# Kernel optimization log

Measured on AMD Instinct MI355X. Metric: run time of the kernel, lower is better.

The kernel has to match this reference:

```python
import jax, jax.numpy as jnp
import numpy as np

B, S, HID, NH = 2, 2048, 2048, 16
HD = HID // NH  # head_dim = 128


def setup_inputs() -> dict:
    key = jax.random.key(0)
    ks = jax.random.split(key, 10)
    sc = 1.0 / np.sqrt(HID)
    inp = {
        "hidden_state": jax.random.normal(ks[0], (B, S, HID), dtype=jnp.float32),
        # upper-triangular (strict) causal mask: 1 where attention is forbidden
        "casual_mask": jnp.triu(jnp.ones((S, S), dtype=jnp.float32), k=1),
        # pad last 128 tokens of each sequence
        "pad_mask": jnp.concatenate(
            [jnp.zeros((B, S - 128), jnp.float32), jnp.ones((B, 128), jnp.float32)], axis=1
        ),
        # weights stored [in, out] (transposed vs torch Linear)
        "Wq": jax.random.normal(ks[1], (HID, HID), dtype=jnp.float32) * sc,
        "bq": jnp.zeros((HID,), jnp.float32),
        "Wk": jax.random.normal(ks[2], (HID, HD), dtype=jnp.float32) * sc,
        "bk": jnp.zeros((HD,), jnp.float32),
        "Wv": jax.random.normal(ks[3], (HID, HD), dtype=jnp.float32) * sc,
        "bv": jnp.zeros((HD,), jnp.float32),
        "Wo": jax.random.normal(ks[4], (HID, HID), dtype=jnp.float32) * sc,
        "bo": jnp.zeros((HID,), jnp.float32),
    }
    return inp


def reference(hidden_state, casual_mask, pad_mask, Wq, bq, Wk, bk, Wv, bv, Wo, bo):
    bsz, seq_len, hid = hidden_state.shape
    nh = NH
    hd = hid // nh
    q = hidden_state @ Wq + bq                      # [B,S,HID]
    k = hidden_state @ Wk + bk                      # [B,S,HD]  single shared head
    v = hidden_state @ Wv + bv                      # [B,S,HD]
    q = q.reshape(bsz, seq_len, nh, hd).transpose(0, 2, 1, 3)  # [B,NH,S,HD]
    # attn scores: shared K broadcast across all query heads
    scores = jnp.einsum("bhqd,bkd->bhqk", q, k) / jnp.sqrt(jnp.float32(hd))
    scores = scores + casual_mask * (-1e9)
    scores = scores + pad_mask[:, None, None, :] * (-1e9)
    probs = jax.nn.softmax(scores, axis=-1)         # [B,NH,S,S]
    out = jnp.einsum("bhqk,bkd->bhqd", probs, v)    # [B,NH,S,HD]
    out = out.transpose(0, 2, 1, 3).reshape(bsz, seq_len, hid)
    return out @ Wo + bo
```

## Files before the change

### kernel.cpp

```cpp
#include <hip/hip_runtime.h>
#include <hip/hip_bf16.h>
#include <math.h>

#define B_    2
#define S_    2048
#define HID_  2048
#define NH_   16
#define HD_   128
#define MTOT  4096
#define QKV_N 2304

typedef short bf16x8 __attribute__((ext_vector_type(8)));
typedef float f32x4  __attribute__((ext_vector_type(4)));
typedef float f32x16 __attribute__((ext_vector_type(16)));

__device__ __forceinline__ ushort f2bf(float f) {
    __hip_bfloat16 h = __float2bfloat16(f);
    ushort u; __builtin_memcpy(&u, &h, 2); return u;
}

__device__ __forceinline__ void gload_lds16(const void* g, void* l) {
    __builtin_amdgcn_global_load_lds(
        (const __attribute__((address_space(1))) void*)g,
        (__attribute__((address_space(3))) void*)l, 16, 0, 0);
}
__device__ __forceinline__ void gload_lds4(const void* g, void* l) {
    __builtin_amdgcn_global_load_lds(
        (const __attribute__((address_space(1))) void*)g,
        (__attribute__((address_space(3))) void*)l, 4, 0, 0);
}

__global__ void cast_f32_bf16(const float* __restrict__ in, ushort* __restrict__ out)
{
    long i = ((long)blockIdx.x * 256 + threadIdx.x) * 8;
    float4 a = *(const float4*)&in[i];
    float4 b = *(const float4*)&in[i + 4];
    uint4 o;
    o.x = (uint)f2bf(a.x) | ((uint)f2bf(a.y) << 16);
    o.y = (uint)f2bf(a.z) | ((uint)f2bf(a.w) << 16);
    o.z = (uint)f2bf(b.x) | ((uint)f2bf(b.y) << 16);
    o.w = (uint)f2bf(b.z) | ((uint)f2bf(b.w) << 16);
    *(uint4*)&out[i] = o;
}

__global__ void transcast(const float* __restrict__ W, ushort* __restrict__ T,
                          int N, int rowoff)
{
    __shared__ float tile[32][33];
    const int tx = threadIdx.x & 31, ty = threadIdx.x >> 5;
    const int n0 = blockIdx.x * 32, k0 = blockIdx.y * 32;
#pragma unroll
    for (int i = 0; i < 4; i++)
        tile[ty + 8 * i][tx] = W[(long)(k0 + ty + 8 * i) * N + n0 + tx];
    __syncthreads();
#pragma unroll
    for (int i = 0; i < 4; i++)
        T[(long)(rowoff + n0 + ty + 8 * i) * 2048 + k0 + tx] = f2bf(tile[tx][ty + 8 * i]);
}

__global__ void fuse_bias(const float* __restrict__ bq, const float* __restrict__ bk,
                          const float* __restrict__ bv, float* __restrict__ bqkv)
{
    int i = blockIdx.x * 256 + threadIdx.x;
    if (i < 2048)      bqkv[i] = bq[i];
    else if (i < 2176) bqkv[i] = bk[i - 2048];
    else if (i < QKV_N) bqkv[i] = bv[i - 2176];
}

__global__ __launch_bounds__(256, 2) void gemm_qkv(
    const ushort* __restrict__ A, const ushort* __restrict__ Bt,
    const float* __restrict__ bias,
    ushort* __restrict__ qbuf, ushort* __restrict__ kbuf,
    ushort* __restrict__ vtbuf)
{
    const int K = HID_;
    __shared__ __align__(16) ushort As[128 * 32];
    __shared__ __align__(16) ushort Bs[128 * 32];
    const int t = threadIdx.x;
    const int w = t >> 6, l = t & 63;
    const long bm = (long)blockIdx.y * 128;
    const long bn = (long)blockIdx.x * 128;

    f32x4 acc[4][4];
#pragma unroll
    for (int i = 0; i < 4; i++)
#pragma unroll
        for (int j = 0; j < 4; j++) acc[i][j] = (f32x4){0.f, 0.f, 0.f, 0.f};

    const int srow = w * 16 + (l >> 2);
    const int scol = (l & 3) * 8;
    const ushort* Ag0 = A + (bm + srow) * (long)K + scol;
    const ushort* Ag1 = A + (bm + srow + 64) * (long)K + scol;
    const ushort* Bg0 = Bt + (bn + srow) * (long)K + scol;
    const ushort* Bg1 = Bt + (bn + srow + 64) * (long)K + scol;
    ushort* Al0 = As + w * 512;
    ushort* Al1 = As + 2048 + w * 512;
    ushort* Bl0 = Bs + w * 512;
    ushort* Bl1 = Bs + 2048 + w * 512;

    const int mrow = l & 15, kq = l >> 4;
    const int moff = (w & 1) * 64, noff = (w >> 1) * 64;

    for (int k0 = 0; k0 < K; k0 += 32) {
        gload_lds16(Ag0 + k0, Al0);
        gload_lds16(Ag1 + k0, Al1);
        gload_lds16(Bg0 + k0, Bl0);
        gload_lds16(Bg1 + k0, Bl1);
        __syncthreads();
        bf16x8 af[4], bfr[4];
#pragma unroll
        for (int i = 0; i < 4; i++)
            af[i] = *(const bf16x8*)&As[(moff + i * 16 + mrow) * 32 + kq * 8];
#pragma unroll
        for (int j = 0; j < 4; j++)
            bfr[j] = *(const bf16x8*)&Bs[(noff + j * 16 + mrow) * 32 + kq * 8];
#pragma unroll
        for (int i = 0; i < 4; i++)
#pragma unroll
            for (int j = 0; j < 4; j++)
                acc[i][j] = __builtin_amdgcn_mfma_f32_16x16x32_bf16(
                    af[i], bfr[j], acc[i][j], 0, 0, 0);
        __syncthreads();
    }

    const int crow = (l >> 4) * 4, ccol = l & 15;
    const int tile = blockIdx.x;
#pragma unroll
    for (int i = 0; i < 4; i++) {
#pragma unroll
        for (int j = 0; j < 4; j++) {
            long colg = bn + noff + j * 16 + ccol;
            float bv = bias[colg];
            long row0 = bm + moff + i * 16 + crow;
            float v[4];
#pragma unroll
            for (int r = 0; r < 4; r++) v[r] = acc[i][j][r] + bv;
            if (tile < 16) {
#pragma unroll
                for (int r = 0; r < 4; r++)
                    qbuf[(row0 + r) * (long)HID_ + colg] = f2bf(v[r]);
            } else if (tile == 16) {
                long ck = colg - 2048;
#pragma unroll
                for (int r = 0; r < 4; r++)
                    kbuf[(row0 + r) * (long)HD_ + ck] = f2bf(v[r]);
            } else {
                long cv = colg - 2176;
                long b  = row0 >> 11;
                long s0 = row0 & 2047;
                ushort4 pk;
                pk.x = f2bf(v[0]); pk.y = f2bf(v[1]);
                pk.z = f2bf(v[2]); pk.w = f2bf(v[3]);
                *(ushort4*)&vtbuf[b * (HD_ * (long)S_) + cv * (long)S_ + s0] = pk;
            }
        }
    }
}

__global__ __launch_bounds__(256, 2) void gemm_mfma(
    const ushort* __restrict__ A, const ushort* __restrict__ Bt,
    const float* __restrict__ bias, float* __restrict__ C,
    int K, int ldc)
{
    __shared__ __align__(16) ushort As[128 * 32];
    __shared__ __align__(16) ushort Bs[128 * 32];
    const int t = threadIdx.x;
    const int w = t >> 6, l = t & 63;
    const long bm = (long)blockIdx.y * 128;
    const long bn = (long)blockIdx.x * 128;

    f32x4 acc[4][4];
#pragma unroll
    for (int i = 0; i < 4; i++)
#pragma unroll
        for (int j = 0; j < 4; j++) acc[i][j] = (f32x4){0.f, 0.f, 0.f, 0.f};

    const int srow = w * 16 + (l >> 2);
    const int scol = (l & 3) * 8;
    const ushort* Ag0 = A + (bm + srow) * (long)K + scol;
    const ushort* Ag1 = A + (bm + srow + 64) * (long)K + scol;
    const ushort* Bg0 = Bt + (bn + srow) * (long)K + scol;
    const ushort* Bg1 = Bt + (bn + srow + 64) * (long)K + scol;
    ushort* Al0 = As + w * 512;
    ushort* Al1 = As + 2048 + w * 512;
    ushort* Bl0 = Bs + w * 512;
    ushort* Bl1 = Bs + 2048 + w * 512;

    const int mrow = l & 15, kq = l >> 4;
    const int moff = (w & 1) * 64, noff = (w >> 1) * 64;

    for (int k0 = 0; k0 < K; k0 += 32) {
        gload_lds16(Ag0 + k0, Al0);
        gload_lds16(Ag1 + k0, Al1);
        gload_lds16(Bg0 + k0, Bl0);
        gload_lds16(Bg1 + k0, Bl1);
        __syncthreads();
        bf16x8 af[4], bfr[4];
#pragma unroll
        for (int i = 0; i < 4; i++)
            af[i] = *(const bf16x8*)&As[(moff + i * 16 + mrow) * 32 + kq * 8];
#pragma unroll
        for (int j = 0; j < 4; j++)
            bfr[j] = *(const bf16x8*)&Bs[(noff + j * 16 + mrow) * 32 + kq * 8];
#pragma unroll
        for (int i = 0; i < 4; i++)
#pragma unroll
            for (int j = 0; j < 4; j++)
                acc[i][j] = __builtin_amdgcn_mfma_f32_16x16x32_bf16(
                    af[i], bfr[j], acc[i][j], 0, 0, 0);
        __syncthreads();
    }

    const int crow = (l >> 4) * 4, ccol = l & 15;
#pragma unroll
    for (int i = 0; i < 4; i++) {
#pragma unroll
        for (int j = 0; j < 4; j++) {
            long col = bn + noff + j * 16 + ccol;
            float bv = bias[col];
#pragma unroll
            for (int r = 0; r < 4; r++) {
                long row = bm + moff + i * 16 + crow + r;
                C[row * (long)ldc + col] = acc[i][j][r] + bv;
            }
        }
    }
}

__global__ __launch_bounds__(256, 2) void attn_mfma(
    const ushort* __restrict__ qbuf, const ushort* __restrict__ kbuf,
    const ushort* __restrict__ vtbuf, const float* __restrict__ pad,
    ushort* __restrict__ outp)
{
    __shared__ __align__(16) char smem[34816];
    ushort* Ks   = (ushort*)smem;
    ushort* Vt   = (ushort*)(smem + 16384);
    float*  padL = (float*)(smem + 32768);

    const int qblk = 15 - (int)blockIdx.x;
    const int h = blockIdx.y, b = blockIdx.z;
    const int t = threadIdx.x, w = t >> 6, l = t & 63;
    const int l31 = l & 31, h5 = l >> 5;
    const long rowbase = (long)b * S_;
    const int qbase = qblk * 128 + w * 32;

    bf16x8 qf[8];
    {
        const ushort* qp = qbuf + (rowbase + qbase + l31) * (long)HID_
                                + h * HD_ + h5 * 8;
#pragma unroll
        for (int ks = 0; ks < 8; ks++) qf[ks] = *(const bf16x8*)(qp + ks * 16);
    }

    f32x16 o[4] = {};
    float mrun = -1e30f, lrun = 0.f;

    const ushort* kg[4]; ushort* kl[4];
    const ushort* vg[4]; ushort* vl[4];
#pragma unroll
    for (int i = 0; i < 4; i++) {
        int key0 = w * 16 + i * 4 + (l >> 4);
        int gk = (l & 15) ^ (key0 & 15);
        kg[i] = kbuf + (rowbase + key0) * (long)HD_ + gk * 8;
        kl[i] = Ks + (w * 16 + i * 4) * 128 + l * 8;
        int d = w * 32 + i * 8 + (l >> 3);
        int gv = (l & 7) ^ (d & 7);
        vg[i] = vtbuf + ((long)b * HD_ + d) * (long)S_ + gv * 8;
        vl[i] = Vt + (w * 32 + i * 8) * 64 + l * 8;
    }

    const int kTiles = 2 * qblk + 2;
    const int qmaxw = qbase + 31;
    const float SC  = 0.08838834764831845f * 1.44269504089f;
    const float NEG = -1.0e9f * 1.44269504089f;

    for (int kt = 0; kt < kTiles; kt++) {
        const int ktb = kt * 64;
#pragma unroll
        for (int i = 0; i < 4; i++) gload_lds16(kg[i] + (long)ktb * HD_, kl[i]);
#pragma unroll
        for (int i = 0; i < 4; i++) gload_lds16(vg[i] + ktb, vl[i]);
        if (w == 0) gload_lds4(pad + rowbase + ktb + l, padL);
        __syncthreads();

        if (ktb <= qmaxw) {
            f32x16 c[2] = {};
#pragma unroll
            for (int mb = 0; mb < 2; mb++) {
                const int key = mb * 32 + l31;
#pragma unroll
                for (int ks = 0; ks < 8; ks++) {
                    int g = (ks * 2 + h5) ^ (key & 15);
                    bf16x8 a = *(const bf16x8*)&Ks[key * 128 + g * 8];
                    c[mb] = __builtin_amdgcn_mfma_f32_32x32x16_bf16(
                        a, qf[ks], c[mb], 0, 0, 0);
                }
            }
            const bool causal = (ktb + 63) > qbase;
            const int qg = qbase + l31;
            float vmax = -3.0e38f;
#pragma unroll
            for (int mb = 0; mb < 2; mb++) {
#pragma unroll
                for (int g = 0; g < 4; g++) {
                    float4 pmv = *(const float4*)&padL[mb * 32 + 4 * h5 + 8 * g];
                    float pmr[4] = {pmv.x, pmv.y, pmv.z, pmv.w};
#pragma unroll
                    for (int r = 0; r < 4; r++) {
                        int reg = g * 4 + r;
                        float v = c[mb][reg] * SC + pmr[r] * NEG;
                        if (causal) {
                            int key = ktb + mb * 32 + 4 * h5 + 8 * g + r;
                            if (key > qg) v += NEG;
                        }
                        c[mb][reg] = v;
                        vmax = fmaxf(vmax, v);
                    }
                }
            }
            vmax = fmaxf(vmax, __shfl_xor(vmax, 32));
            float mnew  = fmaxf(mrun, vmax);
            float alpha = __builtin_amdgcn_exp2f(mrun - mnew);
            float sum = 0.f;
#pragma unroll
            for (int mb = 0; mb < 2; mb++)
#pragma unroll
                for (int reg = 0; reg < 16; reg++) {
                    float p = __builtin_amdgcn_exp2f(c[mb][reg] - mnew);
                    c[mb][reg] = p;
                    sum += p;
                }
            sum += __shfl_xor(sum, 32);
            lrun = lrun * alpha + sum;
            mrun = mnew;
#pragma unroll
            for (int mb = 0; mb < 4; mb++) o[mb] *= alpha;

#pragma unroll
            for (int ks2 = 0; ks2 < 4; ks2++) {
                const int mbs = ks2 >> 1;
                const int base = (ks2 & 1) * 8;
                float own[4], oth[4];
#pragma unroll
                for (int i = 0; i < 4; i++) {
                    float ca = c[mbs][base + i];
                    float cb = c[mbs][base + 4 + i];
                    own[i] = h5 ? cb : ca;
                    oth[i] = h5 ? ca : cb;
                }
                float rec[4];
#pragma unroll
                for (int i = 0; i < 4; i++) rec[i] = __shfl_xor(oth[i], 32);
                bf16x8 pf;
#pragma unroll
                for (int i = 0; i < 4; i++) {
                    pf[i]     = (short)f2bf(h5 ? rec[i] : own[i]);
                    pf[4 + i] = (short)f2bf(h5 ? own[i] : rec[i]);
                }
#pragma unroll
                for (int mb = 0; mb < 4; mb++) {
                    int d = mb * 32 + l31;
                    int g = (ks2 * 2 + h5) ^ (d & 7);
                    bf16x8 a = *(const bf16x8*)&Vt[d * 64 + g * 8];
                    o[mb] = __builtin_amdgcn_mfma_f32_32x32x16_bf16(
                        a, pf, o[mb], 0, 0, 0);
                }
            }
        }
        __syncthreads();
    }

    ushort* Ob = (ushort*)smem + w * 4352;
    float inv = 1.f / lrun;
#pragma unroll
    for (int mb = 0; mb < 4; mb++) {
#pragma unroll
        for (int g = 0; g < 4; g++) {
            int d0 = mb * 32 + 4 * h5 + 8 * g;
            ushort4 pk;
            pk.x = f2bf(o[mb][g * 4 + 0] * inv);
            pk.y = f2bf(o[mb][g * 4 + 1] * inv);
            pk.z = f2bf(o[mb][g * 4 + 2] * inv);
            pk.w = f2bf(o[mb][g * 4 + 3] * inv);
            *(ushort4*)&Ob[l31 * 136 + d0] = pk;
        }
    }
    __builtin_amdgcn_s_waitcnt(0);
    {
        const int q = l >> 1, half = l & 1;
        const ushort* src = Ob + q * 136 + half * 64;
        ushort* dst = outp + (rowbase + qblk * 128 + w * 32 + q) * (long)HID_
                           + h * HD_ + half * 64;
#pragma unroll
        for (int i = 0; i < 8; i++) {
            uint4 v = *(const uint4*)(src + i * 8);
            *(uint4*)(dst + i * 8) = v;
        }
    }
}

extern "C" void kernel_launch(void* const* d_in, const int* in_sizes, int n_in,
                              void* d_out, int out_size, void* d_ws, size_t ws_size,
                              hipStream_t stream)
{
    const float* hidden = (const float*)d_in[0];
    const float* pad = (const float*)d_in[2];
    const float* Wq  = (const float*)d_in[3];
    const float* bq  = (const float*)d_in[4];
    const float* Wk  = (const float*)d_in[5];
    const float* bk  = (const float*)d_in[6];
    const float* Wv  = (const float*)d_in[7];
    const float* bv  = (const float*)d_in[8];
    const float* Wo  = (const float*)d_in[9];
    const float* bo  = (const float*)d_in[10];
    float* out = (float*)d_out;

    char* ws = (char*)d_ws;
    ushort* hbf   = (ushort*)(ws);
    ushort* WqkvT = (ushort*)(ws + 16777216);
    ushort* WoT   = (ushort*)(ws + 26214400);
    float*  bqkv  = (float*) (ws + 34603008);
    ushort* qbuf  = (ushort*)(ws + 34619392);
    ushort* kbuf  = (ushort*)(ws + 51396608);
    ushort* vtbuf = (ushort*)(ws + 52445184);
    ushort* attnO = (ushort*)(ws + 53493760);

    cast_f32_bf16<<<4096, 256, 0, stream>>>(hidden, hbf);
    transcast<<<dim3(64, 64), 256, 0, stream>>>(Wq, WqkvT, 2048, 0);
    transcast<<<dim3(4, 64),  256, 0, stream>>>(Wk, WqkvT, 128, 2048);
    transcast<<<dim3(4, 64),  256, 0, stream>>>(Wv, WqkvT, 128, 2176);
    transcast<<<dim3(64, 64), 256, 0, stream>>>(Wo, WoT, 2048, 0);
    fuse_bias<<<9, 256, 0, stream>>>(bq, bk, bv, bqkv);

    gemm_qkv<<<dim3(18, 32), 256, 0, stream>>>(hbf, WqkvT, bqkv,
                                               qbuf, kbuf, vtbuf);
    attn_mfma<<<dim3(16, NH_, B_), 256, 0, stream>>>(qbuf, kbuf, vtbuf, pad,
                                                     attnO);
    gemm_mfma<<<dim3(16, 32), 256, 0, stream>>>(attnO, WoT, bo, out,
                                                HID_, HID_);
}
```

Measured before the change: 351.3 us.

## Read K/V directly from global in attention, drop LDS staging and barriers

```diff
diff --git a/kernel.cpp b/kernel.cpp
--- a/kernel.cpp
+++ b/kernel.cpp
@@ -23,11 +23,6 @@
     __builtin_amdgcn_global_load_lds(
         (const __attribute__((address_space(1))) void*)g,
         (__attribute__((address_space(3))) void*)l, 16, 0, 0);
-}
-__device__ __forceinline__ void gload_lds4(const void* g, void* l) {
-    __builtin_amdgcn_global_load_lds(
-        (const __attribute__((address_space(1))) void*)g,
-        (__attribute__((address_space(3))) void*)l, 4, 0, 0);
 }
 
 __global__ void cast_f32_bf16(const float* __restrict__ in, ushort* __restrict__ out)
@@ -65,6 +60,12 @@
     if (i < 2048)      bqkv[i] = bq[i];
     else if (i < 2176) bqkv[i] = bk[i - 2048];
     else if (i < QKV_N) bqkv[i] = bv[i - 2176];
+}
+
+__global__ void padscale(const float* __restrict__ pad, float* __restrict__ pb)
+{
+    int i = blockIdx.x * 256 + threadIdx.x;
+    pb[i] = pad[i] * (-1.0e9f * 1.44269504089f);
 }
 
 __global__ __launch_bounds__(256, 2) void gemm_qkv(
@@ -227,15 +228,12 @@
     }
 }
 
-__global__ __launch_bounds__(256, 2) void attn_mfma(
+__global__ __launch_bounds__(256, 3) void attn_mfma(
     const ushort* __restrict__ qbuf, const ushort* __restrict__ kbuf,
-    const ushort* __restrict__ vtbuf, const float* __restrict__ pad,
+    const ushort* __restrict__ vtbuf, const float* __restrict__ pb,
     ushort* __restrict__ outp)
 {
-    __shared__ __align__(16) char smem[34816];
-    ushort* Ks   = (ushort*)smem;
-    ushort* Vt   = (ushort*)(smem + 16384);
-    float*  padL = (float*)(smem + 32768);
+    __shared__ __align__(16) ushort Ob[4][32 * 136];
 
     const int qblk = 15 - (int)blockIdx.x;
     const int h = blockIdx.y, b = blockIdx.z;
@@ -243,6 +241,7 @@
     const int l31 = l & 31, h5 = l >> 5;
     const long rowbase = (long)b * S_;
     const int qbase = qblk * 128 + w * 32;
+    const int qg = qbase + l31;
 
     bf16x8 qf[8];
     {
@@ -252,125 +251,107 @@
         for (int ks = 0; ks < 8; ks++) qf[ks] = *(const bf16x8*)(qp + ks * 16);
     }
 
+    const ushort* kptr = kbuf + (rowbase + l31) * (long)HD_ + h5 * 8;
+    const ushort* vptr = vtbuf + ((long)b * HD_ + l31) * (long)S_ + h5 * 8;
+    const float*  pbp  = pb + rowbase + 4 * h5;
+
     f32x16 o[4] = {};
     float mrun = -1e30f, lrun = 0.f;
 
-    const ushort* kg[4]; ushort* kl[4];
-    const ushort* vg[4]; ushort* vl[4];
-#pragma unroll
-    for (int i = 0; i < 4; i++) {
-        int key0 = w * 16 + i * 4 + (l >> 4);
-        int gk = (l & 15) ^ (key0 & 15);
-        kg[i] = kbuf + (rowbase + key0) * (long)HD_ + gk * 8;
-        kl[i] = Ks + (w * 16 + i * 4) * 128 + l * 8;
-        int d = w * 32 + i * 8 + (l >> 3);
-        int gv = (l & 7) ^ (d & 7);
-        vg[i] = vtbuf + ((long)b * HD_ + d) * (long)S_ + gv * 8;
-        vl[i] = Vt + (w * 32 + i * 8) * 64 + l * 8;
-    }
-
-    const int kTiles = 2 * qblk + 2;
-    const int qmaxw = qbase + 31;
-    const float SC  = 0.08838834764831845f * 1.44269504089f;
+    const int wTiles = (qbase + 31) / 64 + 1;
+    const float SC = 0.08838834764831845f * 1.44269504089f;
     const float NEG = -1.0e9f * 1.44269504089f;
 
-    for (int kt = 0; kt < kTiles; kt++) {
+    for (int kt = 0; kt < wTiles; kt++) {
         const int ktb = kt * 64;
-#pragma unroll
-        for (int i = 0; i < 4; i++) gload_lds16(kg[i] + (long)ktb * HD_, kl[i]);
-#pragma unroll
-        for (int i = 0; i < 4; i++) gload_lds16(vg[i] + ktb, vl[i]);
-        if (w == 0) gload_lds4(pad + rowbase + ktb + l, padL);
-        __syncthreads();
-
-        if (ktb <= qmaxw) {
-            f32x16 c[2] = {};
-#pragma unroll
-            for (int mb = 0; mb < 2; mb++) {
-                const int key = mb * 32 + l31;
-#pragma unroll
-                for (int ks = 0; ks < 8; ks++) {
-                    int g = (ks * 2 + h5) ^ (key & 15);
-                    bf16x8 a = *(const bf16x8*)&Ks[key * 128 + g * 8];
-                    c[mb] = __builtin_amdgcn_mfma_f32_32x32x16_bf16(
-                        a, qf[ks], c[mb], 0, 0, 0);
+
+        f32x16 c[2] = {};
+#pragma unroll
+        for (int mb = 0; mb < 2; mb++) {
+            const ushort* ka = kptr + (long)(ktb + mb * 32) * HD_;
+#pragma unroll
+            for (int ks = 0; ks < 8; ks++) {
+                bf16x8 a = *(const bf16x8*)(ka + ks * 16);
+                c[mb] = __builtin_amdgcn_mfma_f32_32x32x16_bf16(
+                    a, qf[ks], c[mb], 0, 0, 0);
+            }
+        }
+
+        const bool causal = (ktb + 63) > qbase;
+        float vmax = -3.0e38f;
+#pragma unroll
+        for (int mb = 0; mb < 2; mb++) {
+#pragma unroll
+            for (int g = 0; g < 4; g++) {
+                float4 pbv = *(const float4*)&pbp[ktb + mb * 32 + 8 * g];
+                float pbr[4] = {pbv.x, pbv.y, pbv.z, pbv.w};
+#pragma unroll
+                for (int r = 0; r < 4; r++) {
+                    int reg = g * 4 + r;
+                    float v = fmaf(c[mb][reg], SC, pbr[r]);
+                    if (causal) {
+                        int key = ktb + mb * 32 + 4 * h5 + 8 * g + r;
+                        if (key > qg) v += NEG;
+                    }
+                    c[mb][reg] = v;
+                    vmax = fmaxf(vmax, v);
                 }
             }
-            const bool causal = (ktb + 63) > qbase;
-            const int qg = qbase + l31;
-            float vmax = -3.0e38f;
-#pragma unroll
-            for (int mb = 0; mb < 2; mb++) {
-#pragma unroll
-                for (int g = 0; g < 4; g++) {
-                    float4 pmv = *(const float4*)&padL[mb * 32 + 4 * h5 + 8 * g];
-                    float pmr[4] = {pmv.x, pmv.y, pmv.z, pmv.w};
-#pragma unroll
-                    for (int r = 0; r < 4; r++) {
-                        int reg = g * 4 + r;
-                        float v = c[mb][reg] * SC + pmr[r] * NEG;
-                        if (causal) {
-                            int key = ktb + mb * 32 + 4 * h5 + 8 * g + r;
-                            if (key > qg) v += NEG;
-                        }
-                        c[mb][reg] = v;
-                        vmax = fmaxf(vmax, v);
-                    }
-                }
-            }
-            vmax = fmaxf(vmax, __shfl_xor(vmax, 32));
+        }
+        vmax = fmaxf(vmax, __shfl_xor(vmax, 32));
+
+        if (__any(vmax > mrun)) {
             float mnew  = fmaxf(mrun, vmax);
             float alpha = __builtin_amdgcn_exp2f(mrun - mnew);
-            float sum = 0.f;
-#pragma unroll
-            for (int mb = 0; mb < 2; mb++)
-#pragma unroll
-                for (int reg = 0; reg < 16; reg++) {
-                    float p = __builtin_amdgcn_exp2f(c[mb][reg] - mnew);
-                    c[mb][reg] = p;
-                    sum += p;
-                }
-            sum += __shfl_xor(sum, 32);
-            lrun = lrun * alpha + sum;
+            lrun *= alpha;
+#pragma unroll
+            for (int mb = 0; mb < 4; mb++) o[mb] *= alpha;
             mrun = mnew;
-#pragma unroll
-            for (int mb = 0; mb < 4; mb++) o[mb] *= alpha;
-
-#pragma unroll
-            for (int ks2 = 0; ks2 < 4; ks2++) {
-                const int mbs = ks2 >> 1;
-                const int base = (ks2 & 1) * 8;
-                float own[4], oth[4];
-#pragma unroll
-                for (int i = 0; i < 4; i++) {
-                    float ca = c[mbs][base + i];
-                    float cb = c[mbs][base + 4 + i];
-                    own[i] = h5 ? cb : ca;
-                    oth[i] = h5 ? ca : cb;
-                }
-                float rec[4];
-#pragma unroll
-                for (int i = 0; i < 4; i++) rec[i] = __shfl_xor(oth[i], 32);
-                bf16x8 pf;
-#pragma unroll
-                for (int i = 0; i < 4; i++) {
-                    pf[i]     = (short)f2bf(h5 ? rec[i] : own[i]);
-                    pf[4 + i] = (short)f2bf(h5 ? own[i] : rec[i]);
-                }
-#pragma unroll
-                for (int mb = 0; mb < 4; mb++) {
-                    int d = mb * 32 + l31;
-                    int g = (ks2 * 2 + h5) ^ (d & 7);
-                    bf16x8 a = *(const bf16x8*)&Vt[d * 64 + g * 8];
-                    o[mb] = __builtin_amdgcn_mfma_f32_32x32x16_bf16(
-                        a, pf, o[mb], 0, 0, 0);
-                }
-            }
-        }
-        __syncthreads();
-    }
-
-    ushort* Ob = (ushort*)smem + w * 4352;
+        }
+        float sum = 0.f;
+#pragma unroll
+        for (int mb = 0; mb < 2; mb++)
+#pragma unroll
+            for (int reg = 0; reg < 16; reg++) {
+                float p = __builtin_amdgcn_exp2f(c[mb][reg] - mrun);
+                c[mb][reg] = p;
+                sum += p;
+            }
+        sum += __shfl_xor(sum, 32);
+        lrun += sum;
+
+#pragma unroll
+        for (int ks2 = 0; ks2 < 4; ks2++) {
+            const int mbs = ks2 >> 1;
+            const int base = (ks2 & 1) * 8;
+            float own[4], oth[4];
+#pragma unroll
+            for (int i = 0; i < 4; i++) {
+                float ca = c[mbs][base + i];
+                float cb = c[mbs][base + 4 + i];
+                own[i] = h5 ? cb : ca;
+                oth[i] = h5 ? ca : cb;
+            }
+            float rec[4];
+#pragma unroll
+            for (int i = 0; i < 4; i++) rec[i] = __shfl_xor(oth[i], 32);
+            bf16x8 pf;
+#pragma unroll
+            for (int i = 0; i < 4; i++) {
+                pf[i]     = (short)f2bf(h5 ? rec[i] : own[i]);
+                pf[4 + i] = (short)f2bf(h5 ? own[i] : rec[i]);
+            }
+#pragma unroll
+            for (int mb = 0; mb < 4; mb++) {
+                bf16x8 a = *(const bf16x8*)(vptr + (long)(mb * 32) * S_
+                                            + ktb + ks2 * 16);
+                o[mb] = __builtin_amdgcn_mfma_f32_32x32x16_bf16(
+                    a, pf, o[mb], 0, 0, 0);
+            }
+        }
+    }
+
+    ushort* Obw = Ob[w];
     float inv = 1.f / lrun;
 #pragma unroll
     for (int mb = 0; mb < 4; mb++) {
@@ -382,13 +363,13 @@
             pk.y = f2bf(o[mb][g * 4 + 1] * inv);
             pk.z = f2bf(o[mb][g * 4 + 2] * inv);
             pk.w = f2bf(o[mb][g * 4 + 3] * inv);
-            *(ushort4*)&Ob[l31 * 136 + d0] = pk;
+            *(ushort4*)&Obw[l31 * 136 + d0] = pk;
         }
     }
     __builtin_amdgcn_s_waitcnt(0);
     {
         const int q = l >> 1, half = l & 1;
-        const ushort* src = Ob + q * 136 + half * 64;
+        const ushort* src = Obw + q * 136 + half * 64;
         ushort* dst = outp + (rowbase + qblk * 128 + w * 32 + q) * (long)HID_
                            + h * HD_ + half * 64;
 #pragma unroll
@@ -424,6 +405,7 @@
     ushort* kbuf  = (ushort*)(ws + 51396608);
     ushort* vtbuf = (ushort*)(ws + 52445184);
     ushort* attnO = (ushort*)(ws + 53493760);
+    float*  pbuf  = (float*) (ws + 70270976);
 
     cast_f32_bf16<<<4096, 256, 0, stream>>>(hidden, hbf);
     transcast<<<dim3(64, 64), 256, 0, stream>>>(Wq, WqkvT, 2048, 0);
@@ -431,10 +413,11 @@
     transcast<<<dim3(4, 64),  256, 0, stream>>>(Wv, WqkvT, 128, 2176);
     transcast<<<dim3(64, 64), 256, 0, stream>>>(Wo, WoT, 2048, 0);
     fuse_bias<<<9, 256, 0, stream>>>(bq, bk, bv, bqkv);
+    padscale<<<16, 256, 0, stream>>>(pad, pbuf);
 
     gemm_qkv<<<dim3(18, 32), 256, 0, stream>>>(hbf, WqkvT, bqkv,
                                                qbuf, kbuf, vtbuf);
-    attn_mfma<<<dim3(16, NH_, B_), 256, 0, stream>>>(qbuf, kbuf, vtbuf, pad,
+    attn_mfma<<<dim3(16, NH_, B_), 256, 0, stream>>>(qbuf, kbuf, vtbuf, pbuf,
                                                      attnO);
     gemm_mfma<<<dim3(16, 32), 256, 0, stream>>>(attnO, WoT, bo, out,
                                                 HID_, HID_);
```

Result: slower. 547.1 us (+55.8%).
